# Performance work log

Measured on AMD Instinct MI355X. Metric: run time of the kernel, lower is better.

Reference implementation:

```python
import jax, jax.numpy as jnp
import numpy as np

DIM = 512
CODEBOOK_SIZE = 8192
B, N = 8, 2048
EPS = 1e-12


def setup_inputs() -> dict:
    key = jax.random.key(0)
    k1, k2, k3 = jax.random.split(key, 3)
    x = jax.random.normal(k1, (B, N, DIM), dtype=jnp.float32)
    # matches torch.randn(codebook_size, dim) * dim ** -0.5
    codebook = jax.random.normal(k2, (CODEBOOK_SIZE, DIM), dtype=jnp.float32) * DIM ** -0.5
    # nn.Linear(dim, dim, bias=False) weight, applied as x @ W.T
    W = jax.random.normal(k3, (DIM, DIM), dtype=jnp.float32) * DIM ** -0.5
    return {"x": x, "codebook": codebook, "W": W}


def _l2norm(t):
    return t / jnp.maximum(jnp.linalg.norm(t, axis=-1, keepdims=True), EPS)


def _rotate_from_to(q, x):
    """Rotation trick: forward value == q, gradient flows through x via a
    detached Householder-style rotation (R = I - 2ww^T + 2 q_hat x_hat^T)
    and detached norm rescaling."""
    sg = jax.lax.stop_gradient
    norm_x = jnp.linalg.norm(x, axis=-1, keepdims=True)
    norm_q = jnp.linalg.norm(q, axis=-1, keepdims=True)
    x_hat = x / jnp.maximum(norm_x, EPS)
    q_hat = q / jnp.maximum(norm_q, EPS)
    w = sg(_l2norm(x_hat + q_hat))
    x_hat_d, q_hat_d = sg(x_hat), sg(q_hat)
    e = x
    rotated = (e
               - 2.0 * jnp.sum(e * w, axis=-1, keepdims=True) * w
               + 2.0 * jnp.sum(e * x_hat_d, axis=-1, keepdims=True) * q_hat_d)
    return rotated * sg(norm_q / jnp.maximum(norm_x, EPS))


def reference(x, codebook, W):
    # implicit codebook = Linear(codebook)
    codes = jnp.einsum('cd,ed->ce', codebook, W)  # [C, d]
    d2 = -2.0 * jnp.einsum('bnd,cd->bnc', x, codes) + jnp.sum(codes * codes, axis=-1)
    indices = jnp.argmin(jax.lax.stop_gradient(d2), axis=-1)  # [b, n] int
    quantized = codes[indices]  # gather -> [b, n, d]
    commit_loss = jnp.mean((jax.lax.stop_gradient(x) - quantized) ** 2)
    quantized = _rotate_from_to(quantized, x)
    return quantized, indices, commit_loss
```

## Files before the change

### kernel.cpp

```cpp
#include <hip/hip_runtime.h>


#define DIMK  512
#define CBN   8192
#define MROWS 16384

#define SX 24.0f
#define SC 500.0f
#define INV_SS (1.0f / (SX * SC))
#define DKEY  1231
#define NSLOT 3

#define WS_CODES   0UL
#define WS_XQ      16777216UL
#define WS_CQ      25165824UL
#define WS_NORMS   29360128UL
#define WS_CAND    29392896UL
#define WS_CBH     29392896UL
#define WS_CBL     37781504UL
#define WS_WH      54558720UL
#define WS_WL      55083008UL
#define WS_LOSSP   55607296UL

typedef short s16x8 __attribute__((ext_vector_type(8)));
typedef int   i32x4 __attribute__((ext_vector_type(4)));
typedef float f32x4 __attribute__((ext_vector_type(4)));

__device__ __forceinline__ unsigned short f2bf(float f) {
    unsigned u = __float_as_uint(f);
    unsigned r = u + 0x7FFFu + ((u >> 16) & 1u);
    return (unsigned short)(r >> 16);
}
__device__ __forceinline__ float bf2f(unsigned short h) {
    return __uint_as_float(((unsigned)h) << 16);
}
__device__ __forceinline__ void load_lds16(const void* g, void* l) {
    __builtin_amdgcn_global_load_lds((const __attribute__((address_space(1))) void*)g,
                                     (__attribute__((address_space(3))) void*)l,
                                     16, 0, 0);
}
__device__ __forceinline__ signed char q8(float v, float s) {
    return (signed char)__float2int_rn(fminf(fmaxf(v * s, -127.0f), 127.0f));
}

#define WAIT_BAR(N)                                              \
    do {                                                         \
        asm volatile("s_waitcnt vmcnt(" #N ")" ::: "memory");    \
        __builtin_amdgcn_s_barrier();                            \
        asm volatile("" ::: "memory");                           \
    } while (0)

#define DPPX(v, CTRL) \
    ((unsigned)__builtin_amdgcn_update_dpp(0, (int)(v), CTRL, 0xF, 0xF, true))

__global__ __launch_bounds__(256) void prep(
        const float* __restrict__ x, const float* __restrict__ cb, const float* __restrict__ W,
        signed char* __restrict__ xq,
        unsigned short* __restrict__ cbh, unsigned short* __restrict__ cbl,
        unsigned short* __restrict__ wh, unsigned short* __restrict__ wl,
        float* __restrict__ norms) {
    const int b = blockIdx.x;
    const int t = threadIdx.x;
    if (b < 8192) {
        const int i = b * 256 + t;
        float4 v = ((const float4*)x)[i];
        char4 c;
        c.x = q8(v.x, SX); c.y = q8(v.y, SX); c.z = q8(v.z, SX); c.w = q8(v.w, SX);
        ((char4*)xq)[i] = c;
    } else if (b < 12288) {
        const int i = (b - 8192) * 256 + t;
        float4 v = ((const float4*)cb)[i];
        ushort4 h, l;
        h.x = f2bf(v.x); l.x = f2bf(v.x - bf2f(h.x));
        h.y = f2bf(v.y); l.y = f2bf(v.y - bf2f(h.y));
        h.z = f2bf(v.z); l.z = f2bf(v.z - bf2f(h.z));
        h.w = f2bf(v.w); l.w = f2bf(v.w - bf2f(h.w));
        ((ushort4*)cbh)[i] = h;
        ((ushort4*)cbl)[i] = l;
    } else if (b < 12544) {
        const int i = (b - 12288) * 256 + t;
        float4 v = ((const float4*)W)[i];
        ushort4 h, l;
        h.x = f2bf(v.x); l.x = f2bf(v.x - bf2f(h.x));
        h.y = f2bf(v.y); l.y = f2bf(v.y - bf2f(h.y));
        h.z = f2bf(v.z); l.z = f2bf(v.z - bf2f(h.z));
        h.w = f2bf(v.w); l.w = f2bf(v.w - bf2f(h.w));
        ((ushort4*)wh)[i] = h;
        ((ushort4*)wl)[i] = l;
    } else {
        const int i = (b - 12544) * 256 + t;
        norms[i] = 0.0f;
    }
}

__global__ __launch_bounds__(512) void codes_mfma(
        const unsigned short* __restrict__ Ah_g, const unsigned short* __restrict__ Al_g,
        const unsigned short* __restrict__ Bh_g, const unsigned short* __restrict__ Bl_g,
        float* __restrict__ C, signed char* __restrict__ Cq, float* __restrict__ Norms) {
    __shared__ __align__(16) unsigned short Ahi[3][128 * 32];
    __shared__ __align__(16) unsigned short Alo[3][128 * 32];
    __shared__ __align__(16) unsigned short Bhi[3][128 * 32];
    __shared__ __align__(16) unsigned short Blo[3][128 * 32];

    const int t    = threadIdx.x;
    const int w    = t >> 6;
    const int lane = t & 63;
    const int quad = lane >> 4;
    const int l16  = lane & 15;
    const int wm   = w & 3, wn = w >> 2;
    const int rowBase = blockIdx.x * 128;
    const int colBase = blockIdx.y * 128;

    f32x4 acc[2][4];
    #pragma unroll
    for (int i = 0; i < 2; ++i)
        #pragma unroll
        for (int j = 0; j < 4; ++j)
            acc[i][j] = (f32x4)(0.0f);

    const int mr = t >> 2;
    const int kq = ((t & 3) ^ ((t >> 3) & 3)) * 8;
    const size_t gxa = (size_t)(rowBase + mr) * DIMK + kq;
    const size_t gca = (size_t)(colBase + mr) * DIMK + kq;
    const int l0 = w * 512;

    const int swz8 = (quad ^ ((l16 >> 1) & 3)) * 8;

#define CODES_STAGE(B, K0)                                     \
    do {                                                       \
        load_lds16(Ah_g + gxa + (K0), &Ahi[B][l0]);            \
        load_lds16(Al_g + gxa + (K0), &Alo[B][l0]);            \
        load_lds16(Bh_g + gca + (K0), &Bhi[B][l0]);            \
        load_lds16(Bl_g + gca + (K0), &Blo[B][l0]);            \
    } while (0)

#define CODES_COMPUTE(CUR)                                                                         \
    do {                                                                                           \
        s16x8 ah[2], al[2], bh[4], bl[4];                                                          \
        _Pragma("unroll")                                                                          \
        for (int i = 0; i < 2; ++i) {                                                              \
            const int m = wm * 32 + i * 16 + l16;                                                  \
            ah[i] = *(const s16x8*)&Ahi[CUR][m * 32 + swz8];                                       \
            al[i] = *(const s16x8*)&Alo[CUR][m * 32 + swz8];                                       \
        }                                                                                          \
        _Pragma("unroll")                                                                          \
        for (int j = 0; j < 4; ++j) {                                                              \
            const int n = wn * 64 + j * 16 + l16;                                                  \
            bh[j] = *(const s16x8*)&Bhi[CUR][n * 32 + swz8];                                       \
            bl[j] = *(const s16x8*)&Blo[CUR][n * 32 + swz8];                                       \
        }                                                                                          \
        _Pragma("unroll")                                                                          \
        for (int i = 0; i < 2; ++i)                                                                \
            _Pragma("unroll")                                                                      \
            for (int j = 0; j < 4; ++j) {                                                          \
                acc[i][j] = __builtin_amdgcn_mfma_f32_16x16x32_bf16(ah[i], bh[j], acc[i][j], 0, 0, 0); \
                acc[i][j] = __builtin_amdgcn_mfma_f32_16x16x32_bf16(ah[i], bl[j], acc[i][j], 0, 0, 0); \
                acc[i][j] = __builtin_amdgcn_mfma_f32_16x16x32_bf16(al[i], bh[j], acc[i][j], 0, 0, 0); \
            }                                                                                      \
    } while (0)

    CODES_STAGE(0, 0);
    CODES_STAGE(1, 32);
    WAIT_BAR(4);

    CODES_STAGE(2,  64); CODES_COMPUTE(0); WAIT_BAR(4);
    CODES_STAGE(0,  96); CODES_COMPUTE(1); WAIT_BAR(4);
    CODES_STAGE(1, 128); CODES_COMPUTE(2); WAIT_BAR(4);
    CODES_STAGE(2, 160); CODES_COMPUTE(0); WAIT_BAR(4);
    CODES_STAGE(0, 192); CODES_COMPUTE(1); WAIT_BAR(4);
    CODES_STAGE(1, 224); CODES_COMPUTE(2); WAIT_BAR(4);
    CODES_STAGE(2, 256); CODES_COMPUTE(0); WAIT_BAR(4);
    CODES_STAGE(0, 288); CODES_COMPUTE(1); WAIT_BAR(4);
    CODES_STAGE(1, 320); CODES_COMPUTE(2); WAIT_BAR(4);
    CODES_STAGE(2, 352); CODES_COMPUTE(0); WAIT_BAR(4);
    CODES_STAGE(0, 384); CODES_COMPUTE(1); WAIT_BAR(4);
    CODES_STAGE(1, 416); CODES_COMPUTE(2); WAIT_BAR(4);
    CODES_STAGE(2, 448); CODES_COMPUTE(0); WAIT_BAR(4);
    CODES_STAGE(0, 480); CODES_COMPUTE(1); WAIT_BAR(4);
    CODES_COMPUTE(2);                   WAIT_BAR(0);
    CODES_COMPUTE(0);
#undef CODES_STAGE
#undef CODES_COMPUTE

    #pragma unroll
    for (int i = 0; i < 2; ++i) {
        #pragma unroll
        for (int r = 0; r < 4; ++r) {
            const int row = rowBase + wm * 32 + i * 16 + quad * 4 + r;
            float nsum = 0.0f;
            #pragma unroll
            for (int j = 0; j < 4; ++j) {
                const int col = colBase + wn * 64 + j * 16 + l16;
                const float v = acc[i][j][r];
                C[(size_t)row * DIMK + col] = v;
                Cq[(size_t)row * DIMK + col] = q8(v, SC);
                nsum = fmaf(v, v, nsum);
            }
            nsum += __shfl_xor(nsum, 1, 64);
            nsum += __shfl_xor(nsum, 2, 64);
            nsum += __shfl_xor(nsum, 4, 64);
            nsum += __shfl_xor(nsum, 8, 64);
            if (l16 == 0) atomicAdd(&Norms[row], nsum);
        }
    }
}

__global__ __launch_bounds__(512, 6) void d2_argmin_i8(
        const signed char* __restrict__ Xq,
        const signed char* __restrict__ Cq,
        const float* __restrict__ Norms,
        unsigned* __restrict__ Cand) {
    __shared__ __align__(16) signed char Ash[3][128 * 64];
    __shared__ __align__(16) signed char Bsh[3][128 * 64];

    const int t    = threadIdx.x;
    const int w    = t >> 6;
    const int lane = t & 63;
    const int quad = lane >> 4;
    const int l16  = lane & 15;
    const int wm   = w & 3, wn = w >> 2;
    const int rowBase = blockIdx.x * 128;
    const int colBase = blockIdx.y * 128;

    i32x4 acc[2][4];
    #pragma unroll
    for (int i = 0; i < 2; ++i)
        #pragma unroll
        for (int j = 0; j < 4; ++j)
            acc[i][j] = (i32x4)(0);

    const int mr  = t >> 2;
    const int kcs = ((t & 3) ^ ((t >> 3) & 3)) * 16;
    const size_t gxa = (size_t)(rowBase + mr) * DIMK + kcs;
    const size_t gca = (size_t)(colBase + mr) * DIMK + kcs;
    const int lb = w * 1024;

    const int swz  = (quad ^ ((l16 >> 1) & 3)) * 16;
    const int aoff = (wm * 32 + l16) * 64 + swz;
    const int boff = (wn * 64 + l16) * 64 + swz;

    float nq[4];
    #pragma unroll
    for (int j = 0; j < 4; ++j)
        nq[j] = fmaf(Norms[colBase + wn * 64 + j * 16 + l16], 4096.0f, 65536.0f);

#define D2_STAGE(B, K0)                                        \
    do {                                                       \
        load_lds16(Xq + gxa + (K0), &Ash[B][lb]);              \
        load_lds16(Cq + gca + (K0), &Bsh[B][lb]);              \
    } while (0)

#define D2_COMPUTE(CUR)                                                                            \
    do {                                                                                           \
        i32x4 af0 = *(const i32x4*)&Ash[CUR][aoff];                                                \
        i32x4 af1 = *(const i32x4*)&Ash[CUR][aoff + 1024];                                         \
        __builtin_amdgcn_s_setprio(1);                                                             \
        _Pragma("unroll")                                                                          \
        for (int j = 0; j < 4; ++j) {                                                              \
            const i32x4 bfj = *(const i32x4*)&Bsh[CUR][boff + j * 1024];                           \
            acc[0][j] = __builtin_amdgcn_mfma_i32_16x16x64_i8(af0, bfj, acc[0][j], 0, 0, 0);       \
            acc[1][j] = __builtin_amdgcn_mfma_i32_16x16x64_i8(af1, bfj, acc[1][j], 0, 0, 0);       \
        }                                                                                          \
        __builtin_amdgcn_s_setprio(0);                                                             \
    } while (0)

    D2_STAGE(0, 0);
    D2_STAGE(1, 64);
    WAIT_BAR(2);

    D2_STAGE(2, 128); D2_COMPUTE(0); WAIT_BAR(2);
    D2_STAGE(0, 192); D2_COMPUTE(1); WAIT_BAR(2);
    D2_STAGE(1, 256); D2_COMPUTE(2); WAIT_BAR(2);
    D2_STAGE(2, 320); D2_COMPUTE(0); WAIT_BAR(2);
    D2_STAGE(0, 384); D2_COMPUTE(1); WAIT_BAR(2);
    D2_STAGE(1, 448); D2_COMPUTE(2); WAIT_BAR(2);
    D2_COMPUTE(0);                   WAIT_BAR(0);
    D2_COMPUTE(1);
#undef D2_STAGE
#undef D2_COMPUTE

    const unsigned colG = colBase + wn * 64 + l16;
    const int subtile = blockIdx.y * 2 + wn;
    const float C2 = -8192.0f * INV_SS;

    #pragma unroll
    for (int i = 0; i < 2; ++i) {
        #pragma unroll
        for (int r = 0; r < 4; ++r) {
            unsigned k[4];
            #pragma unroll
            for (int j = 0; j < 4; ++j) {
                const float kf = fmaf((float)acc[i][j][r], C2, nq[j]);
                int ki = (int)kf;
                ki = ki < 0 ? 0 : ki;
                ki = ki > 524287 ? 524287 : ki;
                k[j] = ((unsigned)ki << 13) | (colG + j * 16);
            }
            unsigned lo01 = min(k[0], k[1]), hi01 = max(k[0], k[1]);
            unsigned lo23 = min(k[2], k[3]), hi23 = max(k[2], k[3]);
            unsigned a0 = min(lo01, lo23);
            unsigned m  = max(lo01, lo23);
            unsigned tt = min(hi01, hi23);
            unsigned a1 = min(m, tt);
            unsigned a2 = max(m, tt);
#define MERGE_LVL(CTRL)                                           \
            do {                                                  \
                const unsigned b0 = DPPX(a0, CTRL);               \
                const unsigned b1 = DPPX(a1, CTRL);               \
                const unsigned b2 = DPPX(a2, CTRL);               \
                const unsigned M0 = max(a0, b0);                  \
                const unsigned m1 = min(a1, b1);                  \
                a2 = min(max(m1, M0), min(a2, b2));               \
                a1 = min(M0, m1);                                 \
                a0 = min(a0, b0);                                 \
            } while (0)
            MERGE_LVL(0xB1);
            MERGE_LVL(0x4E);
            MERGE_LVL(0x128);
            MERGE_LVL(0x140);
#undef MERGE_LVL
            if (l16 == 0) {
                const int row = rowBase + wm * 32 + i * 16 + quad * 4 + r;
                unsigned* slot = Cand + ((size_t)row * 128 + subtile) * NSLOT;
                slot[0] = a0; slot[1] = a1; slot[2] = a2;
            }
        }
    }
}

__global__ __launch_bounds__(256) void refine_gather(
        const float* __restrict__ X, const float* __restrict__ Codes,
        const float* __restrict__ Norms, const unsigned* __restrict__ Cand,
        float* __restrict__ outQ, float* __restrict__ outIdx,
        float* __restrict__ lossP) {
    const int t    = threadIdx.x;
    const int w    = t >> 6;
    const int lane = t & 63;
    const int row  = blockIdx.x * 4 + w;

    const unsigned* cp = Cand + (size_t)row * 128 * NSLOT + lane * 6;
    unsigned sl[6];
    #pragma unroll
    for (int s = 0; s < 6; ++s) sl[s] = cp[s];

    unsigned mn = sl[0];
    #pragma unroll
    for (int s = 1; s < 6; ++s) mn = min(mn, sl[s]);
    #pragma unroll
    for (int mask = 1; mask < 64; mask <<= 1)
        mn = min(mn, (unsigned)__shfl((int)mn, lane ^ mask, 64));
    const unsigned thrp = (((mn >> 13) + DKEY) << 13) | 0x1FFFu;

    const float4 xa = *(const float4*)(X + (size_t)row * DIMK + lane * 8);
    const float4 xb = *(const float4*)(X + (size_t)row * DIMK + lane * 8 + 4);

    float bestD = __builtin_inff();
    unsigned bestIdx = 0xFFFFFFFFu;

    #pragma unroll
    for (int s = 0; s < 6; ++s) {
        unsigned long long bm = __ballot(sl[s] <= thrp);
        while (bm) {
            const int src = __ffsll(bm) - 1;
            bm &= bm - 1;
            const unsigned sv = (unsigned)__shfl((int)sl[s], src, 64);
            const unsigned idx = sv & 0x1FFFu;
            const float4 ca = *(const float4*)(Codes + (size_t)idx * DIMK + lane * 8);
            const float4 cbv = *(const float4*)(Codes + (size_t)idx * DIMK + lane * 8 + 4);
            float s2 = xa.x * ca.x + xa.y * ca.y + xa.z * ca.z + xa.w * ca.w
                     + xb.x * cbv.x + xb.y * cbv.y + xb.z * cbv.z + xb.w * cbv.w;
            #pragma unroll
            for (int mm = 1; mm < 64; mm <<= 1) s2 += __shfl_xor(s2, mm, 64);
            const float d2 = fmaf(-2.0f, s2, Norms[idx]);
            if (d2 < bestD || (d2 == bestD && idx < bestIdx)) { bestD = d2; bestIdx = idx; }
        }
    }

    const float4 qa = *(const float4*)(Codes + (size_t)bestIdx * DIMK + lane * 8);
    const float4 qb = *(const float4*)(Codes + (size_t)bestIdx * DIMK + lane * 8 + 4);
    *(float4*)(outQ + (size_t)row * DIMK + lane * 8) = qa;
    *(float4*)(outQ + (size_t)row * DIMK + lane * 8 + 4) = qb;
    float dx0 = xa.x - qa.x, dx1 = xa.y - qa.y, dx2 = xa.z - qa.z, dx3 = xa.w - qa.w;
    float dy0 = xb.x - qb.x, dy1 = xb.y - qb.y, dy2 = xb.z - qb.z, dy3 = xb.w - qb.w;
    float s = dx0 * dx0 + dx1 * dx1 + dx2 * dx2 + dx3 * dx3
            + dy0 * dy0 + dy1 * dy1 + dy2 * dy2 + dy3 * dy3;
    #pragma unroll
    for (int off = 32; off > 0; off >>= 1) s += __shfl_down(s, off);
    if (lane == 0) {
        lossP[row] = s;
        outIdx[row] = (float)bestIdx;
    }
}

__global__ __launch_bounds__(1024) void finalize_loss(const float* __restrict__ lossPartials,
                                                      float* __restrict__ outLoss) {
    const int t = threadIdx.x;
    const float4* p = (const float4*)lossPartials;
    const float4 a = p[t];
    const float4 b = p[t + 1024];
    const float4 c = p[t + 2048];
    const float4 d = p[t + 3072];
    float s = (a.x + a.y + a.z + a.w) + (b.x + b.y + b.z + b.w)
            + (c.x + c.y + c.z + c.w) + (d.x + d.y + d.z + d.w);
    #pragma unroll
    for (int off = 32; off > 0; off >>= 1) s += __shfl_down(s, off);
    __shared__ float red[16];
    if ((t & 63) == 0) red[t >> 6] = s;
    __syncthreads();
    if (t < 64) {
        float v = (t < 16) ? red[t] : 0.0f;
        v += __shfl_down(v, 8, 64);
        v += __shfl_down(v, 4, 64);
        v += __shfl_down(v, 2, 64);
        v += __shfl_down(v, 1, 64);
        if (t == 0)
            *outLoss = v * (1.0f / (float)((size_t)MROWS * DIMK));
    }
}

extern "C" void kernel_launch(void* const* d_in, const int* in_sizes, int n_in,
                              void* d_out, int out_size, void* d_ws, size_t ws_size,
                              hipStream_t stream) {
    const float* x  = (const float*)d_in[0];
    const float* cb = (const float*)d_in[1];
    const float* W  = (const float*)d_in[2];
    float* out = (float*)d_out;

    char* ws = (char*)d_ws;
    float* codes          = (float*)(ws + WS_CODES);
    signed char* xq       = (signed char*)(ws + WS_XQ);
    signed char* cq       = (signed char*)(ws + WS_CQ);
    float* norms          = (float*)(ws + WS_NORMS);
    unsigned* cand        = (unsigned*)(ws + WS_CAND);
    unsigned short* cbh   = (unsigned short*)(ws + WS_CBH);
    unsigned short* cbl   = (unsigned short*)(ws + WS_CBL);
    unsigned short* wh    = (unsigned short*)(ws + WS_WH);
    unsigned short* wl    = (unsigned short*)(ws + WS_WL);
    float* lossP          = (float*)(ws + WS_LOSSP);

    prep<<<12576, 256, 0, stream>>>(x, cb, W, xq, cbh, cbl, wh, wl, norms);

    codes_mfma<<<dim3(CBN / 128, DIMK / 128), 512, 0, stream>>>(cbh, cbl, wh, wl, codes, cq, norms);

    d2_argmin_i8<<<dim3(MROWS / 128, CBN / 128), 512, 0, stream>>>(xq, cq, norms, cand);

    refine_gather<<<MROWS / 4, 256, 0, stream>>>(x, codes, norms, cand, out,
                                                 out + (size_t)MROWS * DIMK, lossP);
    finalize_loss<<<1, 1024, 0, stream>>>(lossP, out + (size_t)MROWS * DIMK + MROWS);
}
```

Before: 254.9 us.

## Load A operand directly to registers and double-buffer only B in LDS

The int8 distance GEMM now reads the X-tile fragments straight from global memory into registers, prefetched one k-step ahead, instead of staging them through shared memory. Only the codebook tile stays in LDS, with the pipeline cut from three buffers to two and a plain __syncthreads per step. This lowers LDS footprint and LDS traffic, which may allow more resident blocks. The cost is that each wave issues its own uncoalesced-ish 16-byte global loads for A, with A reuse across the wn waves now served by cache rather than LDS, and the prefetch depth is shallower.

New measurement: 282.0 us. 10.6% more time.

```diff
diff --git a/kernel.cpp b/kernel.cpp
--- a/kernel.cpp
+++ b/kernel.cpp
@@ -210,8 +210,7 @@
         const signed char* __restrict__ Cq,
         const float* __restrict__ Norms,
         unsigned* __restrict__ Cand) {
-    __shared__ __align__(16) signed char Ash[3][128 * 64];
-    __shared__ __align__(16) signed char Bsh[3][128 * 64];
+    __shared__ __align__(16) signed char Bsh[2][128 * 64];
 
     const int t    = threadIdx.x;
     const int w    = t >> 6;
@@ -231,53 +230,59 @@
 
     const int mr  = t >> 2;
     const int kcs = ((t & 3) ^ ((t >> 3) & 3)) * 16;
-    const size_t gxa = (size_t)(rowBase + mr) * DIMK + kcs;
     const size_t gca = (size_t)(colBase + mr) * DIMK + kcs;
     const int lb = w * 1024;
 
     const int swz  = (quad ^ ((l16 >> 1) & 3)) * 16;
-    const int aoff = (wm * 32 + l16) * 64 + swz;
     const int boff = (wn * 64 + l16) * 64 + swz;
+
+    const signed char* pa0 = Xq + (size_t)(rowBase + wm * 32 + l16) * DIMK + quad * 16;
+    const signed char* pa1 = pa0 + (size_t)16 * DIMK;
 
     float nq[4];
     #pragma unroll
     for (int j = 0; j < 4; ++j)
         nq[j] = fmaf(Norms[colBase + wn * 64 + j * 16 + l16], 4096.0f, 65536.0f);
 
-#define D2_STAGE(B, K0)                                        \
-    do {                                                       \
-        load_lds16(Xq + gxa + (K0), &Ash[B][lb]);              \
-        load_lds16(Cq + gca + (K0), &Bsh[B][lb]);              \
-    } while (0)
-
-#define D2_COMPUTE(CUR)                                                                            \
+#define B_STAGE(B, K0) load_lds16(Cq + gca + (K0), &Bsh[B][lb])
+
+#define D2_STEP(CUR, NXT, K0, LAST)                                                                \
     do {                                                                                           \
-        i32x4 af0 = *(const i32x4*)&Ash[CUR][aoff];                                                \
-        i32x4 af1 = *(const i32x4*)&Ash[CUR][aoff + 1024];                                         \
+        i32x4 aN0, aN1;                                                                            \
+        if (!(LAST)) {                                                                             \
+            B_STAGE(NXT, (K0) + 64);                                                               \
+            aN0 = *(const i32x4*)(pa0 + (K0) + 64);                                                \
+            aN1 = *(const i32x4*)(pa1 + (K0) + 64);                                                \
+        }                                                                                          \
         __builtin_amdgcn_s_setprio(1);                                                             \
         _Pragma("unroll")                                                                          \
         for (int j = 0; j < 4; ++j) {                                                              \
             const i32x4 bfj = *(const i32x4*)&Bsh[CUR][boff + j * 1024];                           \
-            acc[0][j] = __builtin_amdgcn_mfma_i32_16x16x64_i8(af0, bfj, acc[0][j], 0, 0, 0);       \
-            acc[1][j] = __builtin_amdgcn_mfma_i32_16x16x64_i8(af1, bfj, acc[1][j], 0, 0, 0);       \
+            acc[0][j] = __builtin_amdgcn_mfma_i32_16x16x64_i8(aC0, bfj, acc[0][j], 0, 0, 0);       \
+            acc[1][j] = __builtin_amdgcn_mfma_i32_16x16x64_i8(aC1, bfj, acc[1][j], 0, 0, 0);       \
         }                                                                                          \
         __builtin_amdgcn_s_setprio(0);                                                             \
+        if (!(LAST)) {                                                                             \
+            __syncthreads();                                                                       \
+            aC0 = aN0; aC1 = aN1;                                                                  \
+        }                                                                                          \
     } while (0)
 
-    D2_STAGE(0, 0);
-    D2_STAGE(1, 64);
-    WAIT_BAR(2);
-
-    D2_STAGE(2, 128); D2_COMPUTE(0); WAIT_BAR(2);
-    D2_STAGE(0, 192); D2_COMPUTE(1); WAIT_BAR(2);
-    D2_STAGE(1, 256); D2_COMPUTE(2); WAIT_BAR(2);
-    D2_STAGE(2, 320); D2_COMPUTE(0); WAIT_BAR(2);
-    D2_STAGE(0, 384); D2_COMPUTE(1); WAIT_BAR(2);
-    D2_STAGE(1, 448); D2_COMPUTE(2); WAIT_BAR(2);
-    D2_COMPUTE(0);                   WAIT_BAR(0);
-    D2_COMPUTE(1);
-#undef D2_STAGE
-#undef D2_COMPUTE
+    B_STAGE(0, 0);
+    i32x4 aC0 = *(const i32x4*)(pa0);
+    i32x4 aC1 = *(const i32x4*)(pa1);
+    __syncthreads();
+
+    D2_STEP(0, 1,   0, false);
+    D2_STEP(1, 0,  64, false);
+    D2_STEP(0, 1, 128, false);
+    D2_STEP(1, 0, 192, false);
+    D2_STEP(0, 1, 256, false);
+    D2_STEP(1, 0, 320, false);
+    D2_STEP(0, 1, 384, false);
+    D2_STEP(1, 0, 448, true);
+#undef D2_STEP
+#undef B_STAGE
 
     const unsigned colG = colBase + wn * 64 + l16;
     const int subtile = blockIdx.y * 2 + wn;
```
